# Kernel tuning notes

Hardware: AMD Instinct MI355X
Metric: run time of the kernel (lower is better)

Reference implementation:

```python
import jax, jax.numpy as jnp
import numpy as np

TAU = 2.0      # membrane time constant
V_TH = 1.0     # spike threshold (v_reset = 0, hard reset)
T_STEPS = 4    # num_steps

@jax.custom_vjp
def heaviside_atan(x):
    # forward: Heaviside; backward: spikingjelly ATan surrogate (alpha=2)
    return (x >= 0.0).astype(x.dtype)

def _h_fwd(x):
    return heaviside_atan(x), x

def _h_bwd(x, g):
    alpha = 2.0
    return (g * (alpha / 2.0) / (1.0 + (jnp.pi / 2.0 * alpha * x) ** 2),)

heaviside_atan.defvjp(_h_fwd, _h_bwd)

def lif_multistep(x_seq):
    # spikingjelly LIFNode, step_mode='m', decay_input=True, v_reset=0, detach_reset=True
    def step(v, x):
        v = v + (x - v) / TAU                      # charge
        s = heaviside_atan(v - V_TH)               # fire (surrogate grad)
        v = v * (1.0 - jax.lax.stop_gradient(s))   # hard reset, detached spike
        return v, s
    v0 = jnp.zeros_like(x_seq[0])
    _, spikes = jax.lax.scan(step, v0, x_seq)
    return spikes

def setup_inputs() -> dict:
    key = jax.random.key(0)
    k0, k1, k2 = jax.random.split(key, 3)
    B, L, C, D, NL = 16, 512, 128, 1024, 2
    inputs = jax.random.normal(k0, (B, L, C), jnp.float32)
    enc_W = jax.random.normal(k1, (C, D), jnp.float32) / np.sqrt(C).astype(np.float32)
    enc_b = jnp.zeros((D,), jnp.float32)
    W_cells = jax.random.normal(k2, (NL, D, D), jnp.float32) / np.sqrt(D).astype(np.float32)
    b_cells = jnp.zeros((NL, D), jnp.float32)
    return {"inputs": inputs, "enc_W": enc_W, "enc_b": enc_b,
            "W_cells": W_cells, "b_cells": b_cells}

def reference(inputs, enc_W, enc_b, W_cells, b_cells):
    # temporal spike encoder: repeat input over T steps, LIF-encode to spikes
    x = jnp.swapaxes(inputs, 1, 2)                       # [B, C, L]
    x = jnp.broadcast_to(x[None], (T_STEPS,) + x.shape)  # [T, B, C, L]
    h = lif_multistep(x)
    h = jnp.swapaxes(h, -2, -1)                          # [T, B, L, C]
    # encoder linear + init LIF
    h = lif_multistep(h @ enc_W + enc_b)                 # [T, B, L, D]
    # stacked SpikeRNNCells: Linear(D,D) -> multistep LIF
    for i in range(W_cells.shape[0]):
        h = lif_multistep(h @ W_cells[i] + b_cells[i])
    out = h.mean(0)                                      # [B, L, D]
    return out, out.mean(axis=1)                         # ([B,L,D], [B,D])
```

## Files before the change

### kernel.cpp

```cpp
#include <hip/hip_runtime.h>
#include <hip/hip_bf16.h>
#include <stdint.h>

#define TSTEPS 4

typedef __bf16 bf16_t;
typedef __attribute__((ext_vector_type(8))) __bf16 bf16x8;
typedef __attribute__((ext_vector_type(16))) float f32x16;
typedef __attribute__((ext_vector_type(4))) unsigned short ushort4v;

union frag_u { bf16x8 v; uint32_t d[4]; unsigned short u[8]; };

#define WT_VM5_LG0  0x075
#define WT_VM4      0xF74
#define WT_VM0_LG0  0x070


__global__ void spike_encode_i8(const float* __restrict__ x,
                                uint4* __restrict__ s1)
{
    const int C = 128;
    int tid = blockIdx.x * blockDim.x + threadIdx.x;
    int row = tid & 31;
    int kb  = (tid >> 5) & 7;
    int m_blk = tid >> 8;
    int m = m_blk * 32 + row;
    const float* px = x + (size_t)m * C + kb * 16;
    float xv[16];
#pragma unroll
    for (int j = 0; j < 16; j += 4) {
        float4 t4 = *(const float4*)(px + j);
        xv[j] = t4.x; xv[j+1] = t4.y; xv[j+2] = t4.z; xv[j+3] = t4.w;
    }
    float v[16];
#pragma unroll
    for (int j = 0; j < 16; ++j) v[j] = 0.0f;
#pragma unroll
    for (int t = 0; t < TSTEPS; ++t) {
        uint32_t dw[4] = {0u, 0u, 0u, 0u};
#pragma unroll
        for (int j = 0; j < 16; ++j) {
            float vv = __fadd_rn(v[j], __fmul_rn(__fsub_rn(xv[j], v[j]), 0.5f));
            bool sp = (vv >= 1.0f);
            dw[j >> 2] |= sp ? (0x3Fu << ((j & 3) * 8)) : 0u;
            v[j] = sp ? 0.0f : vv;
        }
        uint4 o; o.x = dw[0]; o.y = dw[1]; o.z = dw[2]; o.w = dw[3];
        s1[((size_t)(m_blk * 8 + kb) * 4 + t) * 32 + row] = o;
    }
}

__global__ void split_transpose_all(const float* __restrict__ enc_W,
                                    const float* __restrict__ W_cells,
                                    bf16_t* __restrict__ W1h, bf16_t* __restrict__ W1l,
                                    bf16_t* __restrict__ W2h, bf16_t* __restrict__ W2l,
                                    bf16_t* __restrict__ W3h, bf16_t* __restrict__ W3l)
{
    const int N = 1024;
    const float* W;
    bf16_t *hi, *lo;
    int K;
    if (blockIdx.z == 0) {
        if (blockIdx.x >= 4) return;
        W = enc_W; hi = W1h; lo = W1l; K = 128;
    } else if (blockIdx.z == 1) {
        W = W_cells; hi = W2h; lo = W2l; K = 1024;
    } else {
        W = W_cells + (size_t)1024 * 1024; hi = W3h; lo = W3l; K = 1024;
    }
    const int NKB = K >> 4;
    __shared__ float tile[32][33];
    int k0 = blockIdx.x * 32, n0 = blockIdx.y * 32;
    int tx = threadIdx.x & 31, ty = threadIdx.x >> 5;
    for (int kk = ty; kk < 32; kk += 8)
        tile[kk][tx] = W[(size_t)(k0 + kk) * N + n0 + tx];
    __syncthreads();

    const int nn = tx;
    const int oc = ty;
    const int o2 = oc & 3;
    const bool isLo = (oc >> 2) != 0;
    const int kblk = (k0 >> 4) + (o2 >> 1);
    const int lane_in_packet = nn + 32 * (o2 & 1);

    frag_u f;
#pragma unroll
    for (int j = 0; j < 8; ++j) {
        float wv = tile[o2 * 8 + j][nn];
        bf16_t h = (bf16_t)wv;
        bf16_t l = (bf16_t)(wv - (float)h);
        f.v[j] = isLo ? (bf16_t)(2.0f * (float)l)
                      : (bf16_t)(2.0f * (float)h);
    }
    bf16_t* dst = (isLo ? lo : hi)
        + ((size_t)((n0 + nn) >> 5) * NKB + kblk) * 512 + lane_in_packet * 8;
    *(bf16x8*)dst = f.v;
}

template <int K, bool LAST>
__global__ __launch_bounds__(256, 4)
void gemm_lif_mfma(const uint8_t* __restrict__ Abytes,
                   const bf16_t* __restrict__ Bh,
                   const bf16_t* __restrict__ Bl,
                   const float* __restrict__ bias,
                   uint8_t* __restrict__ Sbytes,
                   float* __restrict__ Out,
                   int M, int N)
{
    constexpr int NKB = K >> 4;
    __shared__ __align__(16) uint8_t ldsB[2][4096];
    __shared__ __align__(8) unsigned short sh[4][256];

    const int tid = threadIdx.x;
    const int lane = tid & 63;
    const int wid = tid >> 6;
    const int l31 = lane & 31;
    const int half = lane >> 5;

    const int bid = blockIdx.x;
    const int xcd = bid & 7;
    const int j   = bid >> 3;
    const int nh   = j >> 7;
    const int r    = j & 127;
    const int mloc = r >> 3;
    const int n_t  = nh * 8 + (r & 7);
    const int m_t  = xcd * 16 + mloc;

    const int m0 = m_t * 64, n0 = n_t * 64;
    const int wave_m = (wid & 1) * 32;
    const int wave_n = (wid >> 1) * 32;
    const int m_blk = (m0 + wave_m) >> 5;
    const int n_blk = (n0 + wave_n) >> 5;
    (void)n_blk;

    const uint8_t* pA = Abytes + (size_t)m_blk * NKB * 4 * 512 + l31 * 16 + half * 8;

    const uint8_t* stage_src = (const uint8_t*)(((wid & 1) ? Bl : Bh)
        + (size_t)((n0 >> 5) + (wid >> 1)) * NKB * 512) + (lane << 4);
    const uint8_t* ldsRd = &ldsB[0][0] + ((wid >> 1) << 11) + (lane << 4);

    f32x16 acc[TSTEPS];
#pragma unroll
    for (int t = 0; t < TSTEPS; ++t)
        for (int rr = 0; rr < 16; ++rr) acc[t][rr] = 0.0f;

    uint2 fm[2][4];

#define STAGE(kb_, b_)                                                        \
    __builtin_amdgcn_global_load_lds(                                         \
        (const __attribute__((address_space(1))) uint32_t*)                   \
            (stage_src + (size_t)(kb_) * 1024),                               \
        (__attribute__((address_space(3))) uint32_t*)(&ldsB[b_][wid << 10]),  \
        16, 0, 0);

#define LOADA(kb_, s_) {                                                     \
        fm[s_][0] = *(const uint2*)(pA + ((size_t)(kb_) * 4 + 0) * 512);     \
        fm[s_][1] = *(const uint2*)(pA + ((size_t)(kb_) * 4 + 1) * 512);     \
        fm[s_][2] = *(const uint2*)(pA + ((size_t)(kb_) * 4 + 2) * 512);     \
        fm[s_][3] = *(const uint2*)(pA + ((size_t)(kb_) * 4 + 3) * 512);     \
    }

#define EXPANDF(a_, f_) {                                                    \
        (f_).d[0] = __builtin_amdgcn_perm((a_).x, 0u, 0x05000400u);          \
        (f_).d[1] = __builtin_amdgcn_perm((a_).x, 0u, 0x07000600u);          \
        (f_).d[2] = __builtin_amdgcn_perm((a_).y, 0u, 0x05000400u);          \
        (f_).d[3] = __builtin_amdgcn_perm((a_).y, 0u, 0x07000600u);          \
    }

#define MFMAS(s_, fhv_, flv_) {                                              \
        frag_u af0, af1, af2, af3;                                           \
        EXPANDF(fm[s_][0], af0);                                             \
        EXPANDF(fm[s_][1], af1);                                             \
        EXPANDF(fm[s_][2], af2);                                             \
        EXPANDF(fm[s_][3], af3);                                             \
        acc[0] = __builtin_amdgcn_mfma_f32_32x32x16_bf16(af0.v, fhv_, acc[0], 0, 0, 0); \
        acc[1] = __builtin_amdgcn_mfma_f32_32x32x16_bf16(af1.v, fhv_, acc[1], 0, 0, 0); \
        acc[2] = __builtin_amdgcn_mfma_f32_32x32x16_bf16(af2.v, fhv_, acc[2], 0, 0, 0); \
        acc[3] = __builtin_amdgcn_mfma_f32_32x32x16_bf16(af3.v, fhv_, acc[3], 0, 0, 0); \
        acc[0] = __builtin_amdgcn_mfma_f32_32x32x16_bf16(af0.v, flv_, acc[0], 0, 0, 0); \
        acc[1] = __builtin_amdgcn_mfma_f32_32x32x16_bf16(af1.v, flv_, acc[1], 0, 0, 0); \
        acc[2] = __builtin_amdgcn_mfma_f32_32x32x16_bf16(af2.v, flv_, acc[2], 0, 0, 0); \
        acc[3] = __builtin_amdgcn_mfma_f32_32x32x16_bf16(af3.v, flv_, acc[3], 0, 0, 0); \
    }

#define STEP(kb_, p_) {                                                      \
        STAGE((kb_) + 1, (p_) ^ 1);                                          \
        LOADA((kb_) + 1, (p_) ^ 1);                                          \
        __builtin_amdgcn_s_waitcnt(WT_VM5_LG0);                              \
        asm volatile("" ::: "memory");                                       \
        __builtin_amdgcn_s_setprio(1);                                       \
        MFMAS(p_, cfh, cfl);                                                 \
        __builtin_amdgcn_s_setprio(0);                                       \
        __builtin_amdgcn_s_waitcnt(WT_VM4);                                  \
        asm volatile("" ::: "memory");                                       \
        __builtin_amdgcn_s_barrier();                                        \
        asm volatile("" ::: "memory");                                       \
        cfh = *(const bf16x8*)(ldsRd + (((p_) ^ 1)) * 4096);                 \
        cfl = *(const bf16x8*)(ldsRd + (((p_) ^ 1)) * 4096 + 1024);          \
    }

    STAGE(0, 0);
    LOADA(0, 0);
    __builtin_amdgcn_s_waitcnt(WT_VM4);
    asm volatile("" ::: "memory");
    __builtin_amdgcn_s_barrier();
    asm volatile("" ::: "memory");
    bf16x8 cfh = *(const bf16x8*)(ldsRd);
    bf16x8 cfl = *(const bf16x8*)(ldsRd + 1024);

    for (int kb = 0; kb < NKB - 2; kb += 2) {
        STEP(kb + 0, 0);
        STEP(kb + 1, 1);
    }
    STEP(NKB - 2, 0);
    {
        __builtin_amdgcn_s_waitcnt(WT_VM0_LG0);
        asm volatile("" ::: "memory");
        __builtin_amdgcn_s_setprio(1);
        MFMAS(1, cfh, cfl);
        __builtin_amdgcn_s_setprio(0);
    }

#undef STEP
#undef MFMAS
#undef EXPANDF
#undef LOADA
#undef STAGE

    const float bv = bias[n0 + wave_n + l31];
    f32x16 vmem;
#pragma unroll
    for (int rr = 0; rr < 16; ++rr) vmem[rr] = 0.0f;
    uint64_t bits = 0ull;
    unsigned short* myt = &sh[wid][0];

    const int NKBo = N >> 4;
    const int kbase = (n0 + wave_n) >> 4;

    for (int t = 0; t < TSTEPS; ++t) {
#pragma unroll
        for (int rr = 0; rr < 16; ++rr) {
            float y = __fadd_rn(acc[t][rr], bv);
            float vv = vmem[rr];
            vv = __fadd_rn(vv, __fmul_rn(__fsub_rn(y, vv), 0.5f));
            bool sp = (vv >= 1.0f);
            vmem[rr] = sp ? 0.0f : vv;
            if (LAST) {
                bits |= sp ? (1ull << (rr * 4 + t)) : 0ull;
            } else {
                unsigned long long b = __ballot(sp);
                if (l31 == 0) {
                    uint32_t hb = (uint32_t)(b >> (half * 32));
                    int rowi = (rr & 3) + 8 * (rr >> 2) + 4 * half;
                    myt[(rowi * 2 + 0) * 4 + t] = (unsigned short)hb;
                    myt[(rowi * 2 + 1) * 4 + t] = (unsigned short)(hb >> 16);
                }
            }
        }
    }

    if (LAST) {
        float psum = 0.0f;
#pragma unroll
        for (int rr = 0; rr < 16; ++rr) {
            int m_r = (rr & 3) + 8 * (rr >> 2) + 4 * half;
            int m = m0 + wave_m + m_r;
            int n = n0 + wave_n + l31;
            int cnt = __popc((unsigned)((bits >> (rr * 4)) & 0xFull));
            float val = 0.25f * (float)cnt;
            Out[(size_t)m * N + n] = val;
            psum += val;
        }
        psum += __shfl_xor(psum, 32, 64);
        if (half == 0) {
            float* out2 = Out + (size_t)M * N;
            int b = m0 >> 9;
            int n = n0 + wave_n + l31;
            atomicAdd(out2 + (size_t)b * N + n, psum * (1.0f / 512.0f));
        }
    } else {
        const ushort4v pk = *(const ushort4v*)&myt[(l31 * 2 + half) * 4];
#pragma unroll
        for (int t = 0; t < TSTEPS; ++t) {
            uint32_t m16 = pk[t];
            uint4 o;
            o.x = (((m16      ) & 0xFu) * 0x00204081u & 0x01010101u) * 0x3Fu;
            o.y = (((m16 >>  4) & 0xFu) * 0x00204081u & 0x01010101u) * 0x3Fu;
            o.z = (((m16 >>  8) & 0xFu) * 0x00204081u & 0x01010101u) * 0x3Fu;
            o.w = (((m16 >> 12) & 0xFu) * 0x00204081u & 0x01010101u) * 0x3Fu;
            *(uint4*)(Sbytes + ((((size_t)m_blk * NKBo + kbase + half) * 4 + t)
                                * 32 + l31) * 16) = o;
        }
    }
}

__global__ void zero_out2(float* __restrict__ out2, int n)
{
    int i = blockIdx.x * blockDim.x + threadIdx.x;
    if (i < n) out2[i] = 0.0f;
}

extern "C" void kernel_launch(void* const* d_in, const int* in_sizes, int n_in,
                              void* d_out, int out_size, void* d_ws, size_t ws_size,
                              hipStream_t stream)
{
    const float* inputs  = (const float*)d_in[0];
    const float* enc_W   = (const float*)d_in[1];
    const float* enc_b   = (const float*)d_in[2];
    const float* W_cells = (const float*)d_in[3];
    const float* b_cells = (const float*)d_in[4];

    const int B = 16, L = 512, C = 128, D = 1024;
    const int M = B * L;

    char* ws = (char*)d_ws;
    size_t off = 0;
    uint8_t* s1 = (uint8_t*)(ws + off);
    off += (size_t)(M / 32) * (C / 16) * 4 * 32 * 16;
    bf16_t* W1h = (bf16_t*)(ws + off); off += (size_t)C * D * 2;
    bf16_t* W1l = (bf16_t*)(ws + off); off += (size_t)C * D * 2;
    bf16_t* W2h = (bf16_t*)(ws + off); off += (size_t)D * D * 2;
    bf16_t* W2l = (bf16_t*)(ws + off); off += (size_t)D * D * 2;
    bf16_t* W3h = (bf16_t*)(ws + off); off += (size_t)D * D * 2;
    bf16_t* W3l = (bf16_t*)(ws + off); off += (size_t)D * D * 2;
    uint8_t* h0 = (uint8_t*)(ws + off);
    off += (size_t)(M / 32) * (D / 16) * 4 * 32 * 16;
    uint8_t* h1 = (uint8_t*)(ws + off);

    float* out  = (float*)d_out;
    float* out2 = out + (size_t)M * D;

    split_transpose_all<<<dim3(32, 32, 3), 256, 0, stream>>>(
        enc_W, W_cells, W1h, W1l, W2h, W2l, W3h, W3l);

    spike_encode_i8<<<256, 256, 0, stream>>>(inputs, (uint4*)s1);

    zero_out2<<<(B * D + 255) / 256, 256, 0, stream>>>(out2, B * D);

    const int nblocks = (M / 64) * (D / 64);
    gemm_lif_mfma<128, false><<<nblocks, 256, 0, stream>>>(
        s1, W1h, W1l, enc_b, h0, nullptr, M, D);
    gemm_lif_mfma<1024, false><<<nblocks, 256, 0, stream>>>(
        h0, W2h, W2l, b_cells, h1, nullptr, M, D);
    gemm_lif_mfma<1024, true><<<nblocks, 256, 0, stream>>>(
        h1, W3h, W3l, b_cells + D, nullptr, out, M, D);
}
```

Before: 315.6 us.

## Deepen B-tile LDS prefetch to distance two with four-buffer ring

The B-operand LDS staging moves from a double buffer to a four-slot ring, and global-to-LDS loads are now issued two k-blocks ahead instead of one. This drops the per-step wait for the staging load before the barrier and removes the s_setprio toggles around the MFMA block. The aim is to hide global load latency behind more MFMA work. In exchange LDS use per block grows, which may cut occupancy, and the vmcnt bookkeeping has to stay exactly right.

```diff
diff --git a/kernel.cpp b/kernel.cpp
--- a/kernel.cpp
+++ b/kernel.cpp
@@ -11,8 +11,9 @@
 
 union frag_u { bf16x8 v; uint32_t d[4]; unsigned short u[8]; };
 
+#define WT_VM5      0xF75
 #define WT_VM5_LG0  0x075
-#define WT_VM4      0xF74
+#define WT_VM4_LG0  0x074
 #define WT_VM0_LG0  0x070
 
 
@@ -108,7 +109,7 @@
                    int M, int N)
 {
     constexpr int NKB = K >> 4;
-    __shared__ __align__(16) uint8_t ldsB[2][4096];
+    __shared__ __align__(16) uint8_t ldsB[4][4096];
     __shared__ __align__(8) unsigned short sh[4][256];
 
     const int tid = threadIdx.x;
@@ -130,13 +131,12 @@
     const int wave_m = (wid & 1) * 32;
     const int wave_n = (wid >> 1) * 32;
     const int m_blk = (m0 + wave_m) >> 5;
-    const int n_blk = (n0 + wave_n) >> 5;
-    (void)n_blk;
 
     const uint8_t* pA = Abytes + (size_t)m_blk * NKB * 4 * 512 + l31 * 16 + half * 8;
 
     const uint8_t* stage_src = (const uint8_t*)(((wid & 1) ? Bl : Bh)
         + (size_t)((n0 >> 5) + (wid >> 1)) * NKB * 512) + (lane << 4);
+    uint8_t* ldsStage = &ldsB[0][0] + (wid << 10);
     const uint8_t* ldsRd = &ldsB[0][0] + ((wid >> 1) << 11) + (lane << 4);
 
     f32x16 acc[TSTEPS];
@@ -146,11 +146,12 @@
 
     uint2 fm[2][4];
 
-#define STAGE(kb_, b_)                                                        \
+#define STAGE(kb_, buf_)                                                      \
     __builtin_amdgcn_global_load_lds(                                         \
         (const __attribute__((address_space(1))) uint32_t*)                   \
             (stage_src + (size_t)(kb_) * 1024),                               \
-        (__attribute__((address_space(3))) uint32_t*)(&ldsB[b_][wid << 10]),  \
+        (__attribute__((address_space(3))) uint32_t*)                         \
+            (ldsStage + ((buf_) << 12)),                                      \
         16, 0, 0);
 
 #define LOADA(kb_, s_) {                                                     \
@@ -183,25 +184,22 @@
         acc[3] = __builtin_amdgcn_mfma_f32_32x32x16_bf16(af3.v, flv_, acc[3], 0, 0, 0); \
     }
 
-#define STEP(kb_, p_) {                                                      \
-        STAGE((kb_) + 1, (p_) ^ 1);                                          \
+#define STEPD(kb_, p_) {                                                     \
+        STAGE((kb_) + 2, ((kb_) + 2) & 3);                                   \
         LOADA((kb_) + 1, (p_) ^ 1);                                          \
         __builtin_amdgcn_s_waitcnt(WT_VM5_LG0);                              \
         asm volatile("" ::: "memory");                                       \
-        __builtin_amdgcn_s_setprio(1);                                       \
         MFMAS(p_, cfh, cfl);                                                 \
-        __builtin_amdgcn_s_setprio(0);                                       \
-        __builtin_amdgcn_s_waitcnt(WT_VM4);                                  \
-        asm volatile("" ::: "memory");                                       \
         __builtin_amdgcn_s_barrier();                                        \
         asm volatile("" ::: "memory");                                       \
-        cfh = *(const bf16x8*)(ldsRd + (((p_) ^ 1)) * 4096);                 \
-        cfl = *(const bf16x8*)(ldsRd + (((p_) ^ 1)) * 4096 + 1024);          \
+        cfh = *(const bf16x8*)(ldsRd + ((((kb_) + 1) & 3) << 12));           \
+        cfl = *(const bf16x8*)(ldsRd + ((((kb_) + 1) & 3) << 12) + 1024);    \
     }
 
     STAGE(0, 0);
+    STAGE(1, 1);
     LOADA(0, 0);
-    __builtin_amdgcn_s_waitcnt(WT_VM4);
+    __builtin_amdgcn_s_waitcnt(WT_VM5);
     asm volatile("" ::: "memory");
     __builtin_amdgcn_s_barrier();
     asm volatile("" ::: "memory");
@@ -209,19 +207,22 @@
     bf16x8 cfl = *(const bf16x8*)(ldsRd + 1024);
 
     for (int kb = 0; kb < NKB - 2; kb += 2) {
-        STEP(kb + 0, 0);
-        STEP(kb + 1, 1);
-    }
-    STEP(NKB - 2, 0);
-    {
-        __builtin_amdgcn_s_waitcnt(WT_VM0_LG0);
-        asm volatile("" ::: "memory");
-        __builtin_amdgcn_s_setprio(1);
-        MFMAS(1, cfh, cfl);
-        __builtin_amdgcn_s_setprio(0);
-    }
-
-#undef STEP
+        STEPD(kb + 0, 0);
+        STEPD(kb + 1, 1);
+    }
+    LOADA(NKB - 1, 1);
+    __builtin_amdgcn_s_waitcnt(WT_VM4_LG0);
+    asm volatile("" ::: "memory");
+    MFMAS(0, cfh, cfl);
+    __builtin_amdgcn_s_barrier();
+    asm volatile("" ::: "memory");
+    cfh = *(const bf16x8*)(ldsRd + (((NKB - 1) & 3) << 12));
+    cfl = *(const bf16x8*)(ldsRd + (((NKB - 1) & 3) << 12) + 1024);
+    __builtin_amdgcn_s_waitcnt(WT_VM0_LG0);
+    asm volatile("" ::: "memory");
+    MFMAS(1, cfh, cfl);
+
+#undef STEPD
 #undef MFMAS
 #undef EXPANDF
 #undef LOADA
```

Measured after the change: 303.2 us. -3.9%, faster.
